# Optimization experiments

Hardware: AMD Instinct MI355X
Metric: run time of the kernel (lower is better)

The kernel has to match this reference:

```python
import jax, jax.numpy as jnp
import numpy as np

SEQ, B, V, D, H, R = 256, 64, 10000, 1024, 1024, 2


def setup_inputs() -> dict:
    key = jax.random.key(0)
    ks = jax.random.split(key, 8)
    s = 0.02
    return {
        "tokens": jax.random.randint(ks[0], (SEQ, B), 0, V),           # (seq, batch)
        "emb": jax.random.uniform(ks[1], (V, D), minval=-0.1, maxval=0.1),
        "qw": jax.random.normal(ks[2], (R, D, H)) * s,   # Qw: nhid -> ninp, per mogrify iter
        "qb": jnp.zeros((R, D)),
        "rw": jax.random.normal(ks[3], (R, H, D)) * s,   # Rw: ninp -> nhid
        "rb": jnp.zeros((R, H)),
        "w_ih": jax.random.normal(ks[4], (4 * H, D)) * s,
        "w_hh": jax.random.normal(ks[5], (4 * H, H)) * s,
        "b_ih": jnp.zeros((4 * H,)),
        "b_hh": jnp.zeros((4 * H,)),
        "dec_w": jax.random.uniform(ks[6], (V, H), minval=-0.1, maxval=0.1),
        "dec_b": jnp.zeros((V,)),
        "h0": jnp.zeros((B, H)),
        "c0": jnp.zeros((B, H)),
    }


def reference(tokens, emb, qw, qb, rw, rb, w_ih, w_hh, b_ih, b_hh, dec_w, dec_b, h0, c0):
    def step(carry, tok):
        h, c = carry                      # (B, H), (B, H)
        x = emb[tok]                      # embedding lookup -> (B, D)
        # Mogrify: R alternating gating iterations (dropout=0 / eval mode)
        for r_ in range(R):
            x = 2.0 * jax.nn.sigmoid(h @ qw[r_].T + qb[r_]) * x   # (B, D)
            h = 2.0 * jax.nn.sigmoid(x @ rw[r_].T + rb[r_]) * h   # (B, H)
        # single-layer LSTM cell (PyTorch gate order: i, f, g, o)
        gates = x @ w_ih.T + b_ih + h @ w_hh.T + b_hh              # (B, 4H)
        i, f, g, o = jnp.split(gates, 4, axis=-1)
        c_new = jax.nn.sigmoid(f) * c + jax.nn.sigmoid(i) * jnp.tanh(g)
        h_new = jax.nn.sigmoid(o) * jnp.tanh(c_new)
        dec = h_new @ dec_w.T + dec_b                              # (B, V)
        return (h_new, c_new), dec

    (h_f, c_f), decoded = jax.lax.scan(step, (h0, c0), tokens)     # decoded: (SEQ, B, V)
    return decoded, h_f, c_f
```

## Files before the change

kernel.cpp:

```cpp
#include <hip/hip_runtime.h>
#include <hip/hip_bf16.h>

#define SEQ_LEN 256
#define NB 64
#define NV 10000
#define ND 1024
#define NBLK 256

typedef unsigned int u32;
typedef unsigned short u16;
typedef u32 u32x4 __attribute__((ext_vector_type(4)));
typedef short s16x8 __attribute__((ext_vector_type(8)));
typedef float f32x4 __attribute__((ext_vector_type(4)));

__device__ __forceinline__ float sigf(float z) { return 1.f / (1.f + expf(-z)); }

__device__ __forceinline__ float bflo(u32 u) {
  union { u32 i; float f; } v; v.i = u << 16; return v.f;
}
__device__ __forceinline__ float bfhi(u32 u) {
  union { u32 i; float f; } v; v.i = u & 0xffff0000u; return v.f;
}
__device__ __forceinline__ u16 f2bf(float f) {
  u32 u = __float_as_uint(f);
  u32 r = u + 0x7FFFu + ((u >> 16) & 1u);
  return (u16)(r >> 16);
}

__device__ __forceinline__ u32 ld_uc1(const u32* p) {
  u32 r;
  asm volatile("global_load_dword %0, %1, off sc1\n\ts_waitcnt vmcnt(0)"
               : "=&v"(r) : "v"(p) : "memory");
  return r;
}
__device__ __forceinline__ void st_uc1(u32* p, u32 v) {
  asm volatile("global_store_dword %0, %1, off sc1" :: "v"(p), "v"(v) : "memory");
}
__device__ __forceinline__ void ld_afrag4(const u32* p0, const u32* p1,
                                          const u32* p2, const u32* p3,
                                          u32x4& a0, u32x4& a1, u32x4& a2, u32x4& a3) {
  asm volatile(
      "global_load_dwordx4 %0, %4, off sc1\n\t"
      "global_load_dwordx4 %1, %5, off sc1\n\t"
      "global_load_dwordx4 %2, %6, off sc1\n\t"
      "global_load_dwordx4 %3, %7, off sc1\n\t"
      "s_waitcnt vmcnt(0)"
      : "=&v"(a0), "=&v"(a1), "=&v"(a2), "=&v"(a3)
      : "v"(p0), "v"(p1), "v"(p2), "v"(p3)
      : "memory");
}
__device__ __forceinline__ s16x8 as_frag(u32x4 v) {
  union { u32x4 u; s16x8 s; } c; c.u = v; return c.s;
}

__device__ __forceinline__ float dot8_f32(const float* hv, const float* wp, float acc) {
  float4 w0 = *(const float4*)wp;
  float4 w1 = *(const float4*)(wp + 4);
  acc += hv[0] * w0.x; acc += hv[1] * w0.y; acc += hv[2] * w0.z; acc += hv[3] * w0.w;
  acc += hv[4] * w1.x; acc += hv[5] * w1.y; acc += hv[6] * w1.z; acc += hv[7] * w1.w;
  return acc;
}

__global__ void floodk(float* out, float val, unsigned long long n) {
  unsigned long long i = (unsigned long long)blockIdx.x * 256 + threadIdx.x;
  if (i < n) out[i] = val;
}

__global__ void init_state(const float* __restrict__ h0, const float* __restrict__ c0,
                           float* __restrict__ hT, float* __restrict__ cT,
                           u16* __restrict__ hx16, u32* flags) {
  int i = blockIdx.x * 256 + threadIdx.x;
  int k = i >> 6, b = i & 63;
  float hv = h0[b * ND + k];
  hT[i] = hv;
  cT[i] = c0[b * ND + k];
  hx16[b * ND + k] = f2bf(hv);
  if (i < NBLK * 16) flags[i] = 0u;
}


__device__ __forceinline__ void fbar(u32* flags, u32 want) {
  asm volatile("s_waitcnt vmcnt(0)" ::: "memory");
  __syncthreads();
  const int tid = threadIdx.x;
  if (tid == 0)
    __hip_atomic_store(flags + (size_t)blockIdx.x * 16, want,
                       __ATOMIC_RELAXED, __HIP_MEMORY_SCOPE_AGENT);
  if (tid < 64) {
    for (;;) {
      int ok = 1;
#pragma unroll
      for (int i = 0; i < 4; ++i) {
        u32 f = __hip_atomic_load(flags + (size_t)(tid * 4 + i) * 16,
                                  __ATOMIC_RELAXED, __HIP_MEMORY_SCOPE_AGENT);
        ok &= (f >= want);
      }
      if (__all(ok)) break;
      __builtin_amdgcn_s_sleep(1);
    }
  }
  __syncthreads();
}

template<bool EMB>
__device__ __forceinline__ void mogP(
    const u32* __restrict__ actU, const u16* wAll, int rowbase, const float* bL,
    const float* __restrict__ emb, const int* __restrict__ tok,
    const u32* __restrict__ multU, u32* __restrict__ outU,
    float* red, float* vals2, float* vals)
{
  const int tid = threadIdx.x;
  const int wv = tid >> 6, lane = tid & 63;
  const int c0 = blockIdx.x * 4;
  const int kb = wv * 128;
  const int lm = lane & 15, lh = lane >> 4;
  const u32* ap = actU + (size_t)lm * 512 + (kb >> 1) + lh * 4;
  const int g = rowbase + lm;
  const int swz = (g & 7) << 3;
  f32x4 acc0 = {0.f,0.f,0.f,0.f}, acc1 = acc0, acc2 = acc0, acc3 = acc0;

#pragma unroll
  for (int ks = 0; ks < 4; ++ks) {
    u32x4 a0, a1, a2, a3;
    const u32* p = ap + ks * 16;
    ld_afrag4(p, p + 8192, p + 16384, p + 24576, a0, a1, a2, a3);
    const int e = (kb + ks * 32 + lh * 8) ^ swz;
    s16x8 bf = *(const s16x8*)(wAll + g * 1024 + e);
    acc0 = __builtin_amdgcn_mfma_f32_16x16x32_bf16(as_frag(a0), bf, acc0, 0, 0, 0);
    acc1 = __builtin_amdgcn_mfma_f32_16x16x32_bf16(as_frag(a1), bf, acc1, 0, 0, 0);
    acc2 = __builtin_amdgcn_mfma_f32_16x16x32_bf16(as_frag(a2), bf, acc2, 0, 0, 0);
    acc3 = __builtin_amdgcn_mfma_f32_16x16x32_bf16(as_frag(a3), bf, acc3, 0, 0, 0);
  }
#pragma unroll
  for (int r = 0; r < 4; ++r) {
    red[wv * 1024 + (r     ) * 64 + lane] = acc0[r];
    red[wv * 1024 + (4 + r ) * 64 + lane] = acc1[r];
    red[wv * 1024 + (8 + r ) * 64 + lane] = acc2[r];
    red[wv * 1024 + (12 + r) * 64 + lane] = acc3[r];
  }
  __syncthreads();
  {
    float s0 = 0.f, s1 = 0.f;
#pragma unroll
    for (int w = 0; w < 8; ++w) { s0 += red[w * 1024 + tid]; s1 += red[w * 1024 + 512 + tid]; }
    vals2[tid] = s0; vals2[512 + tid] = s1;
  }
  __syncthreads();

  if (tid < 256) {
    const int c = tid >> 6, b = tid & 63;
    const int i = ((b >> 4) << 2) | (b & 3);
    const int l = (((b >> 2) & 3) << 4) | c;
    float z = vals2[i * 64 + l] + bL[c];
    float g2 = 2.f * sigf(z);
    float m;
    if (EMB) {
      m = emb[(size_t)tok[b] * ND + (c0 + c)];
    } else {
      u32 mu = ld_uc1(multU + (size_t)b * 512 + ((c0 + c) >> 1));
      m = (c & 1) ? bfhi(mu) : bflo(mu);
    }
    vals[c * 64 + b] = g2 * m;
  }
  __syncthreads();

  if (tid < 128) {
    const int cp = tid >> 6, b = tid & 63;
    float lo = vals[(2 * cp) * 64 + b];
    float hi = vals[(2 * cp + 1) * 64 + b];
    u32 pk = (u32)f2bf(lo) | ((u32)f2bf(hi) << 16);
    st_uc1(outU + (size_t)b * 512 + (c0 >> 1) + cp, pk);
  }
}

__device__ __forceinline__ void gatesP(
    const u32* __restrict__ xU, const u32* __restrict__ hU,
    const u16* wAll, const float* bG, float& creg,
    float* __restrict__ hHistN, u32* __restrict__ hxU,
    float* red, float* vals2, float* vals)
{
  const int tid = threadIdx.x;
  const int wv = tid >> 6, lane = tid & 63;
  const int j0 = blockIdx.x * 4;
  const int half = wv >> 2, kq = wv & 3;
  const int kb = kq * 256;
  const int lm = lane & 15, lh = lane >> 4;
  const u32* ap = (half ? hU : xU) + (size_t)lm * 512 + (kb >> 1) + lh * 4;
  const int g = 16 + half * 16 + lm;
  const int swz = (g & 7) << 3;
  f32x4 acc0 = {0.f,0.f,0.f,0.f}, acc1 = acc0, acc2 = acc0, acc3 = acc0;

#pragma unroll
  for (int ks = 0; ks < 8; ++ks) {
    u32x4 a0, a1, a2, a3;
    const u32* p = ap + ks * 16;
    ld_afrag4(p, p + 8192, p + 16384, p + 24576, a0, a1, a2, a3);
    const int e = (kb + ks * 32 + lh * 8) ^ swz;
    s16x8 bf = *(const s16x8*)(wAll + g * 1024 + e);
    acc0 = __builtin_amdgcn_mfma_f32_16x16x32_bf16(as_frag(a0), bf, acc0, 0, 0, 0);
    acc1 = __builtin_amdgcn_mfma_f32_16x16x32_bf16(as_frag(a1), bf, acc1, 0, 0, 0);
    acc2 = __builtin_amdgcn_mfma_f32_16x16x32_bf16(as_frag(a2), bf, acc2, 0, 0, 0);
    acc3 = __builtin_amdgcn_mfma_f32_16x16x32_bf16(as_frag(a3), bf, acc3, 0, 0, 0);
  }
#pragma unroll
  for (int r = 0; r < 4; ++r) {
    red[wv * 1024 + (r     ) * 64 + lane] = acc0[r];
    red[wv * 1024 + (4 + r ) * 64 + lane] = acc1[r];
    red[wv * 1024 + (8 + r ) * 64 + lane] = acc2[r];
    red[wv * 1024 + (12 + r) * 64 + lane] = acc3[r];
  }
  __syncthreads();
  {
    float s0 = 0.f, s1 = 0.f;
#pragma unroll
    for (int w = 0; w < 8; ++w) { s0 += red[w * 1024 + tid]; s1 += red[w * 1024 + 512 + tid]; }
    vals2[tid] = s0; vals2[512 + tid] = s1;
  }
  __syncthreads();

  if (tid < 256) {
    const int jj = tid >> 6, b = tid & 63;
    const int i = ((b >> 4) << 2) | (b & 3);
    const int lbase = (((b >> 2) & 3) << 4);
    float pre[4];
#pragma unroll
    for (int gg = 0; gg < 4; ++gg) {
      const int n = jj * 4 + gg;
      pre[gg] = vals2[i * 64 + (lbase | n)] + bG[n];
    }
    float iv = sigf(pre[0]), fv = sigf(pre[1]);
    float gv = tanhf(pre[2]), ov = sigf(pre[3]);
    float cn = fv * creg + iv * gv;
    creg = cn;
    float hn = ov * tanhf(cn);
    hHistN[(size_t)(j0 + jj) * NB + b] = hn;
    vals[jj * 64 + b] = hn;
  }
  __syncthreads();

  if (tid < 128) {
    const int cp = tid >> 6, b = tid & 63;
    float lo = vals[(2 * cp) * 64 + b];
    float hi = vals[(2 * cp + 1) * 64 + b];
    u32 pk = (u32)f2bf(lo) | ((u32)f2bf(hi) << 16);
    st_uc1(hxU + (size_t)b * 512 + (j0 >> 1) + cp, pk);
  }
}

__global__ __launch_bounds__(512) void seq_kernel(
    const int* __restrict__ tokens, const float* __restrict__ emb,
    const float* __restrict__ qw, const float* __restrict__ qb,
    const float* __restrict__ rw, const float* __restrict__ rb,
    const float* __restrict__ wih, const float* __restrict__ whh,
    const float* __restrict__ bih, const float* __restrict__ bhh,
    u32* __restrict__ hxU, u32* __restrict__ xAU, u32* __restrict__ h1U,
    u32* __restrict__ xBU, u32* __restrict__ h3U,
    float* __restrict__ cS, float* __restrict__ hHist, u32* flags)
{
  __shared__ u16 wAll[48 * 1024];
  __shared__ float red[8 * 1024];
  __shared__ float vals2[1024];
  __shared__ float vals[256];
  __shared__ float bMog[4][4];
  __shared__ float bGs[16];

  const int tid = threadIdx.x;
  const int c0 = blockIdx.x * 4;
  const size_t DH = (size_t)ND * ND;
  const size_t SB = (size_t)ND * NB;

  {
    const float* msrc[4] = {qw, rw, qw + DH, rw + DH};
#pragma unroll
    for (int m = 0; m < 4; ++m)
      for (int c = 0; c < 4; ++c) {
        const int g = m * 4 + c;
        const float* src = msrc[m] + (size_t)(c0 + c) * ND;
        u16* dst = wAll + g * 1024;
        const int swz = (g & 7) << 3;
        for (int k = tid; k < ND; k += 512) dst[k ^ swz] = f2bf(src[k]);
      }
#pragma unroll
    for (int m = 0; m < 2; ++m) {
      const float* W = m ? whh : wih;
      for (int r = 0; r < 16; ++r) {
        const int g = 16 + m * 16 + r;
        const float* src = W + ((size_t)(r & 3) * ND + c0 + (r >> 2)) * ND;
        u16* dst = wAll + g * 1024;
        const int swz = (g & 7) << 3;
        for (int k = tid; k < ND; k += 512) dst[k ^ swz] = f2bf(src[k]);
      }
    }
    if (tid < 16) {
      int p = tid >> 2, c = tid & 3;
      const float* bs = (p == 0) ? qb : (p == 1) ? rb : (p == 2) ? qb + ND : rb + ND;
      bMog[p][c] = bs[c0 + c];
    }
    if (tid >= 16 && tid < 32) {
      int r = tid - 16;
      int jj = r >> 2, g = r & 3;
      bGs[r] = bih[g * ND + c0 + jj] + bhh[g * ND + c0 + jj];
    }
  }
  float creg = 0.f;
  if (tid < 256) creg = cS[(size_t)(c0 + (tid >> 6)) * NB + (tid & 63)];
  __syncthreads();

  u32 want = 0;
  for (int t = 0; t < SEQ_LEN; ++t) {
    const int* tok = tokens + (size_t)t * NB;
    float* hn = hHist + (size_t)(t + 1) * SB;
    mogP<true >(hxU, wAll, 0,  bMog[0], emb, tok, nullptr, xAU, red, vals2, vals); fbar(flags, ++want);
    mogP<false>(xAU, wAll, 4,  bMog[1], nullptr, nullptr, hxU, h1U, red, vals2, vals); fbar(flags, ++want);
    mogP<false>(h1U, wAll, 8,  bMog[2], nullptr, nullptr, xAU, xBU, red, vals2, vals); fbar(flags, ++want);
    mogP<false>(xBU, wAll, 12, bMog[3], nullptr, nullptr, h1U, h3U, red, vals2, vals); fbar(flags, ++want);
    gatesP(xBU, h3U, wAll, bGs, creg, hn, hxU, red, vals2, vals);                      fbar(flags, ++want);
  }
  if (tid < 256) cS[(size_t)(c0 + (tid >> 6)) * NB + (tid & 63)] = creg;
}


template<bool EMB>
__global__ __launch_bounds__(256) void mog_phase(
    const float* __restrict__ actT, const float* __restrict__ W,
    const float* __restrict__ bias, const float* __restrict__ multT,
    const float* __restrict__ emb, const int* __restrict__ tok,
    float* __restrict__ outT)
{
  const int tid = threadIdx.x;
  const int wv = tid >> 6;
  const int lane = tid & 63;
  const int c0 = blockIdx.x * 4;
  __shared__ float red[4][4][64];

  float acc[4] = {0.f, 0.f, 0.f, 0.f};
  const int kb = wv * 256;
  const float* ap = actT + (size_t)kb * NB + lane;

  for (int k = 0; k < 256; k += 8) {
    float hv[8];
#pragma unroll
    for (int q = 0; q < 8; ++q) hv[q] = ap[(k + q) * NB];
#pragma unroll
    for (int c = 0; c < 4; ++c)
      acc[c] = dot8_f32(hv, W + (size_t)(c0 + c) * ND + kb + k, acc[c]);
  }
#pragma unroll
  for (int c = 0; c < 4; ++c) red[wv][c][lane] = acc[c];
  __syncthreads();

  const int c = tid >> 6, b = tid & 63;
  float z = red[0][c][b] + red[1][c][b] + red[2][c][b] + red[3][c][b];
  z += bias[c0 + c];
  float g = 2.f * sigf(z);
  float m;
  if (EMB) m = emb[(size_t)tok[b] * ND + (c0 + c)];
  else     m = multT[(size_t)(c0 + c) * NB + b];
  outT[(size_t)(c0 + c) * NB + b] = g * m;
}

__global__ __launch_bounds__(256) void lstm_gates2(
    const float* __restrict__ xT, const float* __restrict__ hT,
    const float* __restrict__ Wih, const float* __restrict__ Whh,
    const float* __restrict__ bih, const float* __restrict__ bhh,
    float* __restrict__ cT, float* __restrict__ hOut)
{
  const int tid = threadIdx.x;
  const int wv = tid >> 6, lane = tid & 63;
  const int j0 = blockIdx.x * 2;
  __shared__ float red[4][16][64];
  float acc[16];
#pragma unroll
  for (int i = 0; i < 16; ++i) acc[i] = 0.f;
  const int kb = wv * 256;
  const float* xp = xT + (size_t)kb * NB + lane;
  const float* hp = hT + (size_t)kb * NB + lane;

  for (int k = 0; k < 256; k += 8) {
    float xv[8], hv[8];
#pragma unroll
    for (int q = 0; q < 8; ++q) { xv[q] = xp[(k + q) * NB]; hv[q] = hp[(k + q) * NB]; }
#pragma unroll
    for (int jj = 0; jj < 2; ++jj)
#pragma unroll
      for (int g = 0; g < 4; ++g) {
        const size_t row = (size_t)(g * ND + j0 + jj) * ND + kb + k;
        acc[jj * 8 + g]     = dot8_f32(xv, Wih + row, acc[jj * 8 + g]);
        acc[jj * 8 + 4 + g] = dot8_f32(hv, Whh + row, acc[jj * 8 + 4 + g]);
      }
  }
#pragma unroll
  for (int i = 0; i < 16; ++i) red[wv][i][lane] = acc[i];
  __syncthreads();

  if (tid < 128) {
    const int b = tid & 63, jj = tid >> 6;
    const int j = j0 + jj;
    float pre[4];
#pragma unroll
    for (int g = 0; g < 4; ++g) {
      float s = 0.f;
#pragma unroll
      for (int w = 0; w < 4; ++w) s += red[w][jj * 8 + g][b] + red[w][jj * 8 + 4 + g][b];
      pre[g] = s + bih[g * ND + j] + bhh[g * ND + j];
    }
    float iv = sigf(pre[0]), fv = sigf(pre[1]);
    float gv = tanhf(pre[2]), ov = sigf(pre[3]);
    float cn = fv * cT[(size_t)j * NB + b] + iv * gv;
    float hn = ov * tanhf(cn);
    cT[(size_t)j * NB + b] = cn;
    hOut[(size_t)j * NB + b] = hn;
  }
}

__global__ __launch_bounds__(256) void decode_k(
    const float* __restrict__ hT, const float* __restrict__ W,
    const float* __restrict__ decb, float* __restrict__ out)
{
  const int tid = threadIdx.x;
  const int wv = tid >> 6, lane = tid & 63;
  const int v0 = blockIdx.x * 4;
  __shared__ float red[4][4][64];
  float acc[4] = {0.f, 0.f, 0.f, 0.f};
  const int kb = wv * 256;
  const float* hp = hT + (size_t)kb * NB + lane;

  for (int k = 0; k < 256; k += 8) {
    float hv[8];
#pragma unroll
    for (int q = 0; q < 8; ++q) hv[q] = hp[(k + q) * NB];
#pragma unroll
    for (int c = 0; c < 4; ++c)
      acc[c] = dot8_f32(hv, W + (size_t)(v0 + c) * ND + kb + k, acc[c]);
  }
#pragma unroll
  for (int c = 0; c < 4; ++c) red[wv][c][lane] = acc[c];
  __syncthreads();

  const int c = tid >> 6, b = tid & 63;
  float z = red[0][c][b] + red[1][c][b] + red[2][c][b] + red[3][c][b];
  z += decb[v0 + c];
  out[(size_t)b * NV + v0 + c] = z;
}

__global__ __launch_bounds__(256) void decode_gemm(
    const float* __restrict__ A,
    const float* __restrict__ Bw,
    const float* __restrict__ bias,
    float* __restrict__ C)
{
  const int tid = threadIdx.x;
  const int bid = blockIdx.x;
  const int mt = bid & 255;
  const int nt = bid >> 8;
  const int n0 = nt * 64;

  __shared__ float As[2048];
  __shared__ float Bs[2048];

  const int tm = tid >> 4, tn = tid & 15;
  float acc[4][4] = {{0.f}};
  const float* Abase = A + (size_t)mt * (ND * NB);

  for (int k0 = 0; k0 < ND; k0 += 32) {
    __syncthreads();
    {
      const float4* src = (const float4*)(Abase + (size_t)k0 * NB);
      ((float4*)As)[tid] = src[tid];
      ((float4*)As)[tid + 256] = src[tid + 256];
    }
#pragma unroll
    for (int i = 0; i < 2; ++i) {
      int f = tid + i * 256;
      int n = f >> 3;
      int kc = f & 7;
      int gn = n0 + n;
      float4 v = make_float4(0.f, 0.f, 0.f, 0.f);
      if (gn < NV) v = *(const float4*)(Bw + (size_t)gn * ND + k0 + kc * 4);
      int k = kc * 4;
      int n4 = n >> 2, nr = n & 3;
      Bs[(k + 0) * 64 + ((n4 ^ ((k + 0) & 7)) << 2) + nr] = v.x;
      Bs[(k + 1) * 64 + ((n4 ^ ((k + 1) & 7)) << 2) + nr] = v.y;
      Bs[(k + 2) * 64 + ((n4 ^ ((k + 2) & 7)) << 2) + nr] = v.z;
      Bs[(k + 3) * 64 + ((n4 ^ ((k + 3) & 7)) << 2) + nr] = v.w;
    }
    __syncthreads();
#pragma unroll
    for (int kk = 0; kk < 32; ++kk) {
      float a4[4], b4[4];
      *(float4*)a4 = *(const float4*)(As + kk * 64 + tm * 4);
      *(float4*)b4 = *(const float4*)(Bs + kk * 64 + ((tn ^ (kk & 7)) << 2));
#pragma unroll
      for (int i = 0; i < 4; ++i)
#pragma unroll
        for (int j = 0; j < 4; ++j)
          acc[i][j] = fmaf(a4[i], b4[j], acc[i][j]);
    }
  }

  const int nb = n0 + tn * 4;
  float db[4];
#pragma unroll
  for (int j = 0; j < 4; ++j) db[j] = (nb + j < NV) ? bias[nb + j] : 0.f;
  float* Crow = C + (size_t)mt * ((size_t)NB * NV);
#pragma unroll
  for (int i = 0; i < 4; ++i) {
    const int b = tm * 4 + i;
    float* cp = Crow + (size_t)b * NV + nb;
    if (nb + 3 < NV) {
      float4 v;
      v.x = acc[i][0] + db[0]; v.y = acc[i][1] + db[1];
      v.z = acc[i][2] + db[2]; v.w = acc[i][3] + db[3];
      *(float4*)cp = v;
    } else {
#pragma unroll
      for (int j = 0; j < 4; ++j)
        if (nb + j < NV) cp[j] = acc[i][j] + db[j];
    }
  }
}

__global__ void finalize(const float* __restrict__ hT, const float* __restrict__ cT,
                         float* __restrict__ out) {
  int i = blockIdx.x * 256 + threadIdx.x;
  int k = i >> 6, b = i & 63;
  size_t base = (size_t)SEQ_LEN * NB * NV;
  out[base + (size_t)b * ND + k] = hT[i];
  out[base + (size_t)NB * ND + (size_t)b * ND + k] = cT[i];
}

extern "C" void kernel_launch(void* const* d_in, const int* in_sizes, int n_in,
                              void* d_out, int out_size, void* d_ws, size_t ws_size,
                              hipStream_t stream)
{
  float* out = (float*)d_out;
  const unsigned long long expect_out = (unsigned long long)SEQ_LEN * NB * NV + 2ull * NB * ND;

  auto flood = [&](float v) {
    unsigned long long n = (unsigned long long)out_size;
    unsigned int g = (unsigned int)((n + 255) / 256);
    floodk<<<g, 256, 0, stream>>>(out, v, n);
  };
  const int expect_sz[14] = {
    SEQ_LEN * NB, NV * ND, 2 * ND * ND, 2 * ND, 2 * ND * ND, 2 * ND,
    4 * ND * ND, 4 * ND * ND, 4 * ND, 4 * ND, NV * ND, NV, NB * ND, NB * ND };
  if (n_in != 14) { flood(1000.f); return; }
  for (int i = 0; i < 14; ++i)
    if (in_sizes[i] != expect_sz[i]) { flood(1100.f + 100.f * i); return; }
  if ((unsigned long long)out_size != expect_out) { flood(2500.f); return; }

  float* ws = (float*)d_ws;
  const size_t SB = (size_t)ND * NB;
  if (ws_size < 7 * SB * sizeof(float)) { flood(2600.f); return; }

  const int*   tokens = (const int*)d_in[0];
  const float* emb  = (const float*)d_in[1];
  const float* qw   = (const float*)d_in[2];
  const float* qb   = (const float*)d_in[3];
  const float* rw   = (const float*)d_in[4];
  const float* rb   = (const float*)d_in[5];
  const float* wih  = (const float*)d_in[6];
  const float* whh  = (const float*)d_in[7];
  const float* bih  = (const float*)d_in[8];
  const float* bhh  = (const float*)d_in[9];
  const float* decw = (const float*)d_in[10];
  const float* decb = (const float*)d_in[11];
  const float* h0   = (const float*)d_in[12];
  const float* c0   = (const float*)d_in[13];

  float* cS    = ws;
  float* hHist = ws + SB;
  u32*   ex    = (u32*)(ws + SB + (size_t)(SEQ_LEN + 1) * SB);
  const size_t EXB = 64 * 512;
  u32* hxU = ex + 0 * EXB;
  u32* xAU = ex + 1 * EXB;
  u32* h1U = ex + 2 * EXB;
  u32* xBU = ex + 3 * EXB;
  u32* h3U = ex + 4 * EXB;
  u32* flags = ex + 5 * EXB;

  const size_t DH = (size_t)ND * ND;
  const size_t need = ((size_t)(1 + SEQ_LEN + 1) * SB) * sizeof(float)
                    + (5 * EXB + NBLK * 16) * sizeof(u32);
  const bool big = ws_size >= need;

  if (big) {
    init_state<<<256, 256, 0, stream>>>(h0, c0, hHist, cS, (u16*)hxU, flags);
    seq_kernel<<<NBLK, 512, 0, stream>>>(tokens, emb, qw, qb, rw, rb,
                                         wih, whh, bih, bhh,
                                         hxU, xAU, h1U, xBU, h3U,
                                         cS, hHist, flags);
    decode_gemm<<<157 * 256, 256, 0, stream>>>(hHist + SB, decw, decb, out);
    finalize<<<256, 256, 0, stream>>>(hHist + (size_t)SEQ_LEN * SB, cS, out);
  } else {
    float* xA = ws + 0 * SB;
    float* xB = ws + 1 * SB;
    float* h1 = ws + 2 * SB;
    float* h3 = ws + 3 * SB;
    float* cSf = ws + 4 * SB;
    float* hA = ws + 5 * SB;
    float* hB = ws + 6 * SB;
    u32* fdummy = (u32*)(ws + 6 * SB);
    init_state<<<256, 256, 0, stream>>>(h0, c0, hA, cSf, (u16*)hB, fdummy);
    float* hc = hA;
    float* hn = hB;
    for (int t = 0; t < SEQ_LEN; ++t) {
      const int* tk = tokens + (size_t)t * NB;
      mog_phase<true ><<<256, 256, 0, stream>>>(hc, qw, qb, nullptr, emb, tk, xA);
      mog_phase<false><<<256, 256, 0, stream>>>(xA, rw, rb, hc, nullptr, nullptr, h1);
      mog_phase<false><<<256, 256, 0, stream>>>(h1, qw + DH, qb + ND, xA, nullptr, nullptr, xB);
      mog_phase<false><<<256, 256, 0, stream>>>(xB, rw + DH, rb + ND, h1, nullptr, nullptr, h3);
      lstm_gates2<<<512, 256, 0, stream>>>(xB, h3, wih, whh, bih, bhh, cSf, hn);
      decode_k<<<2500, 256, 0, stream>>>(hn, decw, decb, out + (size_t)t * NB * NV);
      float* tmp = hc; hc = hn; hn = tmp;
    }
    finalize<<<256, 256, 0, stream>>>(hc, cSf, out);
  }
}
```

Measured before the change: 16.00 ms.

## Move decoder GEMM to bf16 MFMA and batch activation loads in persistent kernel

Replaces the fp32 FMA decoder GEMM with a bf16 MFMA kernel. It reads a bf16 hidden-state history written directly by the recurrent kernel and a bf16 copy of the decoder weights made by a new conversion kernel. Inside the persistent sequence kernel, all A-fragment loads for a phase are issued before a single wait, and the multiplier load is hoisted ahead of the MFMAs, to hide global latency. The grid-barrier flags are packed contiguously so each poll is one vector load. The trade-off is bf16 rounding in the decoder, an extra weight-conversion pass, and higher register pressure.

Measured after the change: 16.14 ms. Within noise of the previous version (+0.9%).

```diff
diff --git a/kernel.cpp b/kernel.cpp
--- a/kernel.cpp
+++ b/kernel.cpp
@@ -4,6 +4,7 @@
 #define SEQ_LEN 256
 #define NB 64
 #define NV 10000
+#define NVP 10048
 #define ND 1024
 #define NBLK 256
 
@@ -27,27 +28,23 @@
   return (u16)(r >> 16);
 }
 
-__device__ __forceinline__ u32 ld_uc1(const u32* p) {
-  u32 r;
-  asm volatile("global_load_dword %0, %1, off sc1\n\ts_waitcnt vmcnt(0)"
-               : "=&v"(r) : "v"(p) : "memory");
-  return r;
-}
 __device__ __forceinline__ void st_uc1(u32* p, u32 v) {
   asm volatile("global_store_dword %0, %1, off sc1" :: "v"(p), "v"(v) : "memory");
 }
-__device__ __forceinline__ void ld_afrag4(const u32* p0, const u32* p1,
-                                          const u32* p2, const u32* p3,
-                                          u32x4& a0, u32x4& a1, u32x4& a2, u32x4& a3) {
+__device__ __forceinline__ void ld_a4_issue(const u32* p, u32x4& a0, u32x4& a1,
+                                            u32x4& a2, u32x4& a3) {
   asm volatile(
       "global_load_dwordx4 %0, %4, off sc1\n\t"
-      "global_load_dwordx4 %1, %5, off sc1\n\t"
-      "global_load_dwordx4 %2, %6, off sc1\n\t"
-      "global_load_dwordx4 %3, %7, off sc1\n\t"
-      "s_waitcnt vmcnt(0)"
+      "global_load_dwordx4 %1, %4, off offset:64 sc1\n\t"
+      "global_load_dwordx4 %2, %4, off offset:128 sc1\n\t"
+      "global_load_dwordx4 %3, %4, off offset:192 sc1"
       : "=&v"(a0), "=&v"(a1), "=&v"(a2), "=&v"(a3)
-      : "v"(p0), "v"(p1), "v"(p2), "v"(p3)
+      : "v"(p)
       : "memory");
+}
+__device__ __forceinline__ void wait_vm0() {
+  asm volatile("s_waitcnt vmcnt(0)" ::: "memory");
+  __builtin_amdgcn_sched_barrier(0);
 }
 __device__ __forceinline__ s16x8 as_frag(u32x4 v) {
   union { u32x4 u; s16x8 s; } c; c.u = v; return c.s;
@@ -67,15 +64,30 @@
 }
 
 __global__ void init_state(const float* __restrict__ h0, const float* __restrict__ c0,
-                           float* __restrict__ hT, float* __restrict__ cT,
-                           u16* __restrict__ hx16, u32* flags) {
+                           float* __restrict__ cS, u16* __restrict__ hx16, u32* flags) {
   int i = blockIdx.x * 256 + threadIdx.x;
   int k = i >> 6, b = i & 63;
-  float hv = h0[b * ND + k];
-  hT[i] = hv;
-  cT[i] = c0[b * ND + k];
-  hx16[b * ND + k] = f2bf(hv);
-  if (i < NBLK * 16) flags[i] = 0u;
+  cS[i] = c0[b * ND + k];
+  hx16[b * ND + k] = f2bf(h0[b * ND + k]);
+  if (i < NBLK) flags[i] = 0u;
+}
+
+__global__ void cvt_dec(const float* __restrict__ decw, u16* __restrict__ Wb) {
+  size_t i = (size_t)blockIdx.x * 256 + threadIdx.x;
+  size_t base = i * 8;
+  if (base >= (size_t)NVP * ND) return;
+  size_t row = base >> 10;
+  ushort4 o0, o1;
+  if (row < NV) {
+    float4 v0 = *(const float4*)(decw + base);
+    float4 v1 = *(const float4*)(decw + base + 4);
+    o0 = make_ushort4(f2bf(v0.x), f2bf(v0.y), f2bf(v0.z), f2bf(v0.w));
+    o1 = make_ushort4(f2bf(v1.x), f2bf(v1.y), f2bf(v1.z), f2bf(v1.w));
+  } else {
+    o0 = make_ushort4(0, 0, 0, 0); o1 = o0;
+  }
+  *(ushort4*)(Wb + base) = o0;
+  *(ushort4*)(Wb + base + 4) = o1;
 }
 
 
@@ -84,17 +96,15 @@
   __syncthreads();
   const int tid = threadIdx.x;
   if (tid == 0)
-    __hip_atomic_store(flags + (size_t)blockIdx.x * 16, want,
+    __hip_atomic_store(flags + blockIdx.x, want,
                        __ATOMIC_RELAXED, __HIP_MEMORY_SCOPE_AGENT);
   if (tid < 64) {
+    const u32* fp = flags + tid * 4;
     for (;;) {
-      int ok = 1;
-#pragma unroll
-      for (int i = 0; i < 4; ++i) {
-        u32 f = __hip_atomic_load(flags + (size_t)(tid * 4 + i) * 16,
-                                  __ATOMIC_RELAXED, __HIP_MEMORY_SCOPE_AGENT);
-        ok &= (f >= want);
-      }
+      u32x4 f;
+      asm volatile("global_load_dwordx4 %0, %1, off sc1\n\ts_waitcnt vmcnt(0)"
+                   : "=&v"(f) : "v"(fp) : "memory");
+      int ok = (f[0] >= want) & (f[1] >= want) & (f[2] >= want) & (f[3] >= want);
       if (__all(ok)) break;
       __builtin_amdgcn_s_sleep(1);
     }
@@ -117,27 +127,37 @@
   const u32* ap = actU + (size_t)lm * 512 + (kb >> 1) + lh * 4;
   const int g = rowbase + lm;
   const int swz = (g & 7) << 3;
-  f32x4 acc0 = {0.f,0.f,0.f,0.f}, acc1 = acc0, acc2 = acc0, acc3 = acc0;
-
-#pragma unroll
-  for (int ks = 0; ks < 4; ++ks) {
-    u32x4 a0, a1, a2, a3;
-    const u32* p = ap + ks * 16;
-    ld_afrag4(p, p + 8192, p + 16384, p + 24576, a0, a1, a2, a3);
-    const int e = (kb + ks * 32 + lh * 8) ^ swz;
-    s16x8 bf = *(const s16x8*)(wAll + g * 1024 + e);
-    acc0 = __builtin_amdgcn_mfma_f32_16x16x32_bf16(as_frag(a0), bf, acc0, 0, 0, 0);
-    acc1 = __builtin_amdgcn_mfma_f32_16x16x32_bf16(as_frag(a1), bf, acc1, 0, 0, 0);
-    acc2 = __builtin_amdgcn_mfma_f32_16x16x32_bf16(as_frag(a2), bf, acc2, 0, 0, 0);
-    acc3 = __builtin_amdgcn_mfma_f32_16x16x32_bf16(as_frag(a3), bf, acc3, 0, 0, 0);
-  }
-#pragma unroll
-  for (int r = 0; r < 4; ++r) {
-    red[wv * 1024 + (r     ) * 64 + lane] = acc0[r];
-    red[wv * 1024 + (4 + r ) * 64 + lane] = acc1[r];
-    red[wv * 1024 + (8 + r ) * 64 + lane] = acc2[r];
-    red[wv * 1024 + (12 + r) * 64 + lane] = acc3[r];
-  }
+
+  u32x4 A[4][4];
+#pragma unroll
+  for (int m = 0; m < 4; ++m)
+    ld_a4_issue(ap + m * 8192, A[m][0], A[m][1], A[m][2], A[m][3]);
+  u32 mu = 0;
+  if (!EMB && tid < 256) {
+    const int ec = tid >> 6, eb = tid & 63;
+    const u32* mp = multU + (size_t)eb * 512 + ((c0 + ec) >> 1);
+    asm volatile("global_load_dword %0, %1, off sc1" : "=&v"(mu) : "v"(mp) : "memory");
+  }
+  s16x8 bf[4];
+#pragma unroll
+  for (int ks = 0; ks < 4; ++ks)
+    bf[ks] = *(const s16x8*)(wAll + g * 1024 + ((kb + ks * 32 + lh * 8) ^ swz));
+  wait_vm0();
+
+  f32x4 acc[4];
+#pragma unroll
+  for (int m = 0; m < 4; ++m) { acc[m] = (f32x4){0.f,0.f,0.f,0.f}; }
+#pragma unroll
+  for (int ks = 0; ks < 4; ++ks)
+#pragma unroll
+    for (int m = 0; m < 4; ++m)
+      acc[m] = __builtin_amdgcn_mfma_f32_16x16x32_bf16(as_frag(A[m][ks]), bf[ks], acc[m], 0, 0, 0);
+
+#pragma unroll
+  for (int m = 0; m < 4; ++m)
+#pragma unroll
+    for (int r = 0; r < 4; ++r)
+      red[wv * 1024 + (m * 4 + r) * 64 + lane] = acc[m][r];
   __syncthreads();
   {
     float s0 = 0.f, s1 = 0.f;
@@ -154,12 +174,8 @@
     float z = vals2[i * 64 + l] + bL[c];
     float g2 = 2.f * sigf(z);
     float m;
-    if (EMB) {
-      m = emb[(size_t)tok[b] * ND + (c0 + c)];
-    } else {
-      u32 mu = ld_uc1(multU + (size_t)b * 512 + ((c0 + c) >> 1));
-      m = (c & 1) ? bfhi(mu) : bflo(mu);
-    }
+    if (EMB) m = emb[(size_t)tok[b] * ND + (c0 + c)];
+    else     m = (c & 1) ? bfhi(mu) : bflo(mu);
     vals[c * 64 + b] = g2 * m;
   }
   __syncthreads();
@@ -176,7 +192,7 @@
 __device__ __forceinline__ void gatesP(
     const u32* __restrict__ xU, const u32* __restrict__ hU,
     const u16* wAll, const float* bG, float& creg,
-    float* __restrict__ hHistN, u32* __restrict__ hxU,
+    u32* __restrict__ hBrow, u32* __restrict__ hxU, float* __restrict__ hFw,
     float* red, float* vals2, float* vals)
 {
   const int tid = threadIdx.x;
@@ -188,27 +204,33 @@
   const u32* ap = (half ? hU : xU) + (size_t)lm * 512 + (kb >> 1) + lh * 4;
   const int g = 16 + half * 16 + lm;
   const int swz = (g & 7) << 3;
-  f32x4 acc0 = {0.f,0.f,0.f,0.f}, acc1 = acc0, acc2 = acc0, acc3 = acc0;
-
-#pragma unroll
-  for (int ks = 0; ks < 8; ++ks) {
-    u32x4 a0, a1, a2, a3;
-    const u32* p = ap + ks * 16;
-    ld_afrag4(p, p + 8192, p + 16384, p + 24576, a0, a1, a2, a3);
-    const int e = (kb + ks * 32 + lh * 8) ^ swz;
-    s16x8 bf = *(const s16x8*)(wAll + g * 1024 + e);
-    acc0 = __builtin_amdgcn_mfma_f32_16x16x32_bf16(as_frag(a0), bf, acc0, 0, 0, 0);
-    acc1 = __builtin_amdgcn_mfma_f32_16x16x32_bf16(as_frag(a1), bf, acc1, 0, 0, 0);
-    acc2 = __builtin_amdgcn_mfma_f32_16x16x32_bf16(as_frag(a2), bf, acc2, 0, 0, 0);
-    acc3 = __builtin_amdgcn_mfma_f32_16x16x32_bf16(as_frag(a3), bf, acc3, 0, 0, 0);
-  }
-#pragma unroll
-  for (int r = 0; r < 4; ++r) {
-    red[wv * 1024 + (r     ) * 64 + lane] = acc0[r];
-    red[wv * 1024 + (4 + r ) * 64 + lane] = acc1[r];
-    red[wv * 1024 + (8 + r ) * 64 + lane] = acc2[r];
-    red[wv * 1024 + (12 + r) * 64 + lane] = acc3[r];
-  }
+
+  u32x4 A[4][8];
+#pragma unroll
+  for (int m = 0; m < 4; ++m) {
+    ld_a4_issue(ap + m * 8192,      A[m][0], A[m][1], A[m][2], A[m][3]);
+    ld_a4_issue(ap + m * 8192 + 64, A[m][4], A[m][5], A[m][6], A[m][7]);
+  }
+  s16x8 bf[8];
+#pragma unroll
+  for (int ks = 0; ks < 8; ++ks)
+    bf[ks] = *(const s16x8*)(wAll + g * 1024 + ((kb + ks * 32 + lh * 8) ^ swz));
+  wait_vm0();
+
+  f32x4 acc[4];
+#pragma unroll
+  for (int m = 0; m < 4; ++m) { acc[m] = (f32x4){0.f,0.f,0.f,0.f}; }
+#pragma unroll
+  for (int ks = 0; ks < 8; ++ks)
+#pragma unroll
+    for (int m = 0; m < 4; ++m)
+      acc[m] = __builtin_amdgcn_mfma_f32_16x16x32_bf16(as_frag(A[m][ks]), bf[ks], acc[m], 0, 0, 0);
+
+#pragma unroll
+  for (int m = 0; m < 4; ++m)
+#pragma unroll
+    for (int r = 0; r < 4; ++r)
+      red[wv * 1024 + (m * 4 + r) * 64 + lane] = acc[m][r];
   __syncthreads();
   {
     float s0 = 0.f, s1 = 0.f;
@@ -233,8 +255,8 @@
     float cn = fv * creg + iv * gv;
     creg = cn;
     float hn = ov * tanhf(cn);
-    hHistN[(size_t)(j0 + jj) * NB + b] = hn;
     vals[jj * 64 + b] = hn;
+    if (hFw) hFw[(size_t)(j0 + jj) * NB + b] = hn;
   }
   __syncthreads();
 
@@ -243,7 +265,8 @@
     float lo = vals[(2 * cp) * 64 + b];
     float hi = vals[(2 * cp + 1) * 64 + b];
     u32 pk = (u32)f2bf(lo) | ((u32)f2bf(hi) << 16);
-    st_uc1(hxU + (size_t)b * 512 + (j0 >> 1) + cp, pk);
+    st_uc1(hxU + (size_t)b * 512 + (blockIdx.x * 2) + cp, pk);
+    hBrow[(size_t)b * 512 + (blockIdx.x * 2) + cp] = pk;
   }
 }
 
@@ -255,7 +278,8 @@
     const float* __restrict__ bih, const float* __restrict__ bhh,
     u32* __restrict__ hxU, u32* __restrict__ xAU, u32* __restrict__ h1U,
     u32* __restrict__ xBU, u32* __restrict__ h3U,
-    float* __restrict__ cS, float* __restrict__ hHist, u32* flags)
+    float* __restrict__ cS, u32* __restrict__ hB, float* __restrict__ hF,
+    u32* flags)
 {
   __shared__ u16 wAll[48 * 1024];
   __shared__ float red[8 * 1024];
@@ -267,7 +291,6 @@
   const int tid = threadIdx.x;
   const int c0 = blockIdx.x * 4;
   const size_t DH = (size_t)ND * ND;
-  const size_t SB = (size_t)ND * NB;
 
   {
     const float* msrc[4] = {qw, rw, qw + DH, rw + DH};
@@ -309,16 +332,78 @@
   u32 want = 0;
   for (int t = 0; t < SEQ_LEN; ++t) {
     const int* tok = tokens + (size_t)t * NB;
-    float* hn = hHist + (size_t)(t + 1) * SB;
+    u32* hBrow = hB + (size_t)t * 32768;
+    float* hFw = (t == SEQ_LEN - 1) ? hF : nullptr;
     mogP<true >(hxU, wAll, 0,  bMog[0], emb, tok, nullptr, xAU, red, vals2, vals); fbar(flags, ++want);
     mogP<false>(xAU, wAll, 4,  bMog[1], nullptr, nullptr, hxU, h1U, red, vals2, vals); fbar(flags, ++want);
     mogP<false>(h1U, wAll, 8,  bMog[2], nullptr, nullptr, xAU, xBU, red, vals2, vals); fbar(flags, ++want);
     mogP<false>(xBU, wAll, 12, bMog[3], nullptr, nullptr, h1U, h3U, red, vals2, vals); fbar(flags, ++want);
-    gatesP(xBU, h3U, wAll, bGs, creg, hn, hxU, red, vals2, vals);                      fbar(flags, ++want);
+    gatesP(xBU, h3U, wAll, bGs, creg, hBrow, hxU, hFw, red, vals2, vals);              fbar(flags, ++want);
   }
   if (tid < 256) cS[(size_t)(c0 + (tid >> 6)) * NB + (tid & 63)] = creg;
 }
 
+__global__ __launch_bounds__(256) void decode_mfma(
+    const u32* __restrict__ hB,
+    const u16* __restrict__ Wb,
+    const float* __restrict__ bias,
+    float* __restrict__ out)
+{
+  int bid = blockIdx.x;
+  bid = (bid & 7) * (NBLK * 157 / 8) + (bid >> 3);
+  const int mt = bid / 157;
+  const int nt = bid % 157;
+  const int tid = threadIdx.x;
+  const int wv = tid >> 6, lane = tid & 63;
+  const int lm = lane & 15, lh = lane >> 4;
+  const int n = nt * 64 + wv * 16 + lm;
+  const u16* bp = Wb + (size_t)n * 1024 + lh * 8;
+  const u32* ap = hB + (size_t)mt * 32768 + (size_t)lm * 512 + lh * 4;
+
+  f32x4 acc[4];
+#pragma unroll
+  for (int m = 0; m < 4; ++m) acc[m] = (f32x4){0.f, 0.f, 0.f, 0.f};
+
+#pragma unroll 4
+  for (int ks = 0; ks < 32; ++ks) {
+    s16x8 bf = *(const s16x8*)(bp + ks * 32);
+#pragma unroll
+    for (int m = 0; m < 4; ++m) {
+      u32x4 av = *(const u32x4*)(ap + m * 8192 + ks * 16);
+      acc[m] = __builtin_amdgcn_mfma_f32_16x16x32_bf16(as_frag(av), bf, acc[m], 0, 0, 0);
+    }
+  }
+
+  const float db = (n < NV) ? bias[n] : 0.f;
+  float* orow = out + (size_t)mt * NB * NV + n;
+  if (n < NV) {
+#pragma unroll
+    for (int m = 0; m < 4; ++m)
+#pragma unroll
+      for (int r = 0; r < 4; ++r) {
+        const int b = m * 16 + lh * 4 + r;
+        orow[(size_t)b * NV] = acc[m][r] + db;
+      }
+  }
+}
+
+__global__ void finalize(const float* __restrict__ hT, const float* __restrict__ cT,
+                         float* __restrict__ out) {
+  int i = blockIdx.x * 256 + threadIdx.x;
+  int k = i >> 6, b = i & 63;
+  size_t base = (size_t)SEQ_LEN * NB * NV;
+  out[base + (size_t)b * ND + k] = hT[i];
+  out[base + (size_t)NB * ND + (size_t)b * ND + k] = cT[i];
+}
+
+
+__global__ void init_state_fb(const float* __restrict__ h0, const float* __restrict__ c0,
+                              float* __restrict__ hT, float* __restrict__ cT) {
+  int i = blockIdx.x * 256 + threadIdx.x;
+  int k = i >> 6, b = i & 63;
+  hT[i] = h0[b * ND + k];
+  cT[i] = c0[b * ND + k];
+}
 
 template<bool EMB>
 __global__ __launch_bounds__(256) void mog_phase(
@@ -441,92 +526,6 @@
   float z = red[0][c][b] + red[1][c][b] + red[2][c][b] + red[3][c][b];
   z += decb[v0 + c];
   out[(size_t)b * NV + v0 + c] = z;
-}
-
-__global__ __launch_bounds__(256) void decode_gemm(
-    const float* __restrict__ A,
-    const float* __restrict__ Bw,
-    const float* __restrict__ bias,
-    float* __restrict__ C)
-{
-  const int tid = threadIdx.x;
-  const int bid = blockIdx.x;
-  const int mt = bid & 255;
-  const int nt = bid >> 8;
-  const int n0 = nt * 64;
-
-  __shared__ float As[2048];
-  __shared__ float Bs[2048];
-
-  const int tm = tid >> 4, tn = tid & 15;
-  float acc[4][4] = {{0.f}};
-  const float* Abase = A + (size_t)mt * (ND * NB);
-
-  for (int k0 = 0; k0 < ND; k0 += 32) {
-    __syncthreads();
-    {
-      const float4* src = (const float4*)(Abase + (size_t)k0 * NB);
-      ((float4*)As)[tid] = src[tid];
-      ((float4*)As)[tid + 256] = src[tid + 256];
-    }
-#pragma unroll
-    for (int i = 0; i < 2; ++i) {
-      int f = tid + i * 256;
-      int n = f >> 3;
-      int kc = f & 7;
-      int gn = n0 + n;
-      float4 v = make_float4(0.f, 0.f, 0.f, 0.f);
-      if (gn < NV) v = *(const float4*)(Bw + (size_t)gn * ND + k0 + kc * 4);
-      int k = kc * 4;
-      int n4 = n >> 2, nr = n & 3;
-      Bs[(k + 0) * 64 + ((n4 ^ ((k + 0) & 7)) << 2) + nr] = v.x;
-      Bs[(k + 1) * 64 + ((n4 ^ ((k + 1) & 7)) << 2) + nr] = v.y;
-      Bs[(k + 2) * 64 + ((n4 ^ ((k + 2) & 7)) << 2) + nr] = v.z;
-      Bs[(k + 3) * 64 + ((n4 ^ ((k + 3) & 7)) << 2) + nr] = v.w;
-    }
-    __syncthreads();
-#pragma unroll
-    for (int kk = 0; kk < 32; ++kk) {
-      float a4[4], b4[4];
-      *(float4*)a4 = *(const float4*)(As + kk * 64 + tm * 4);
-      *(float4*)b4 = *(const float4*)(Bs + kk * 64 + ((tn ^ (kk & 7)) << 2));
-#pragma unroll
-      for (int i = 0; i < 4; ++i)
-#pragma unroll
-        for (int j = 0; j < 4; ++j)
-          acc[i][j] = fmaf(a4[i], b4[j], acc[i][j]);
-    }
-  }
-
-  const int nb = n0 + tn * 4;
-  float db[4];
-#pragma unroll
-  for (int j = 0; j < 4; ++j) db[j] = (nb + j < NV) ? bias[nb + j] : 0.f;
-  float* Crow = C + (size_t)mt * ((size_t)NB * NV);
-#pragma unroll
-  for (int i = 0; i < 4; ++i) {
-    const int b = tm * 4 + i;
-    float* cp = Crow + (size_t)b * NV + nb;
-    if (nb + 3 < NV) {
-      float4 v;
-      v.x = acc[i][0] + db[0]; v.y = acc[i][1] + db[1];
-      v.z = acc[i][2] + db[2]; v.w = acc[i][3] + db[3];
-      *(float4*)cp = v;
-    } else {
-#pragma unroll
-      for (int j = 0; j < 4; ++j)
-        if (nb + j < NV) cp[j] = acc[i][j] + db[j];
-    }
-  }
-}
-
-__global__ void finalize(const float* __restrict__ hT, const float* __restrict__ cT,
-                         float* __restrict__ out) {
-  int i = blockIdx.x * 256 + threadIdx.x;
-  int k = i >> 6, b = i & 63;
-  size_t base = (size_t)SEQ_LEN * NB * NV;
-  out[base + (size_t)b * ND + k] = hT[i];
-  out[base + (size_t)NB * ND + (size_t)b * ND + k] = cT[i];
 }
 
 extern "C" void kernel_launch(void* const* d_in, const int* in_sizes, int n_in,
@@ -569,8 +568,10 @@
   const float* c0   = (const float*)d_in[13];
 
   float* cS    = ws;
-  float* hHist = ws + SB;
-  u32*   ex    = (u32*)(ws + SB + (size_t)(SEQ_LEN + 1) * SB);
+  float* hF    = ws + SB;
+  u32*   hB    = (u32*)(ws + 2 * SB);
+  u16*   decwB = (u16*)(hB + (size_t)SEQ_LEN * 32768);
+  u32*   ex    = (u32*)(decwB + (size_t)NVP * ND);
   const size_t EXB = 64 * 512;
   u32* hxU = ex + 0 * EXB;
   u32* xAU = ex + 1 * EXB;
@@ -580,18 +581,21 @@
   u32* flags = ex + 5 * EXB;
 
   const size_t DH = (size_t)ND * ND;
-  const size_t need = ((size_t)(1 + SEQ_LEN + 1) * SB) * sizeof(float)
-                    + (5 * EXB + NBLK * 16) * sizeof(u32);
+  const size_t need = 2 * SB * sizeof(float)
+                    + (size_t)SEQ_LEN * 32768 * sizeof(u32)
+                    + (size_t)NVP * ND * sizeof(u16)
+                    + (5 * EXB + NBLK) * sizeof(u32);
   const bool big = ws_size >= need;
 
   if (big) {
-    init_state<<<256, 256, 0, stream>>>(h0, c0, hHist, cS, (u16*)hxU, flags);
+    init_state<<<256, 256, 0, stream>>>(h0, c0, cS, (u16*)hxU, flags);
+    cvt_dec<<<(NVP * ND / 8 + 255) / 256, 256, 0, stream>>>(decw, decwB);
     seq_kernel<<<NBLK, 512, 0, stream>>>(tokens, emb, qw, qb, rw, rb,
                                          wih, whh, bih, bhh,
                                          hxU, xAU, h1U, xBU, h3U,
-                                         cS, hHist, flags);
-    decode_gemm<<<157 * 256, 256, 0, stream>>>(hHist + SB, decw, decb, out);
-    finalize<<<256, 256, 0, stream>>>(hHist + (size_t)SEQ_LEN * SB, cS, out);
+                                         cS, hB, hF, flags);
+    decode_mfma<<<NBLK * 157, 256, 0, stream>>>(hB, decwB, decb, out);
+    finalize<<<256, 256, 0, stream>>>(hF, cS, out);
   } else {
     float* xA = ws + 0 * SB;
     float* xB = ws + 1 * SB;
@@ -599,11 +603,10 @@
     float* h3 = ws + 3 * SB;
     float* cSf = ws + 4 * SB;
     float* hA = ws + 5 * SB;
-    float* hB = ws + 6 * SB;
-    u32* fdummy = (u32*)(ws + 6 * SB);
-    init_state<<<256, 256, 0, stream>>>(h0, c0, hA, cSf, (u16*)hB, fdummy);
+    float* hBf = ws + 6 * SB;
+    init_state_fb<<<256, 256, 0, stream>>>(h0, c0, hA, cSf);
     float* hc = hA;
-    float* hn = hB;
+    float* hn = hBf;
     for (int t = 0; t < SEQ_LEN; ++t) {
       const int* tk = tokens + (size_t)t * NB;
       mog_phase<true ><<<256, 256, 0, stream>>>(hc, qw, qb, nullptr, emb, tk, xA);
```
